# Kernel optimization log

Measured on AMD Instinct MI355X. Metric: run time of the kernel, lower is better.

Reference implementation:

```python
import jax, jax.numpy as jnp
import numpy as np

N = 100000   # nodes
E = 1600000  # edges
F = 128      # input node features
H = 128      # hidden channels
G = 512      # graphs in batch
EPS = 1e-5   # BatchNorm eps


def setup_inputs() -> dict:
    key = jax.random.key(0)
    ks = jax.random.split(key, 24)
    x = jax.random.normal(ks[0], (N, F), jnp.float32)
    edge_index = jax.random.randint(ks[1], (2, E), 0, N)
    batch = jnp.sort(jax.random.randint(ks[2], (N,), 0, G))

    def lin_w(k, i, o):
        return jax.random.normal(k, (i, o), jnp.float32) / np.sqrt(i)

    inp = {
        "x": x, "edge_index": edge_index, "batch": batch,
        "W1": lin_w(ks[3], F, H), "b1": jnp.zeros((H,), jnp.float32),
        "g1": jnp.ones((H,), jnp.float32), "be1": jnp.zeros((H,), jnp.float32),
        "m1": 0.1 * jax.random.normal(ks[4], (H,), jnp.float32),
        "v1": jax.random.uniform(ks[5], (H,), jnp.float32) + 0.5,
        "W2": lin_w(ks[6], H, H), "b2": jnp.zeros((H,), jnp.float32),
        "g2": jnp.ones((H,), jnp.float32), "be2": jnp.zeros((H,), jnp.float32),
        "m2": 0.1 * jax.random.normal(ks[7], (H,), jnp.float32),
        "v2": jax.random.uniform(ks[8], (H,), jnp.float32) + 0.5,
        "W3": lin_w(ks[9], H, H), "b3": jnp.zeros((H,), jnp.float32),
        "g3": jnp.ones((H,), jnp.float32), "be3": jnp.zeros((H,), jnp.float32),
        "m3": 0.1 * jax.random.normal(ks[10], (H,), jnp.float32),
        "v3": jax.random.uniform(ks[11], (H,), jnp.float32) + 0.5,
        "Wl": lin_w(ks[12], H, 1), "bl": jnp.zeros((1,), jnp.float32),
    }
    return inp


def _gcn_norm(edge_index):
    # add self-loops, then symmetric normalization deg^-1/2 A_hat deg^-1/2
    loops = jnp.arange(N)
    src = jnp.concatenate([edge_index[0], loops])
    dst = jnp.concatenate([edge_index[1], loops])
    deg = jax.ops.segment_sum(jnp.ones_like(src, jnp.float32), dst, num_segments=N)
    dinv = jax.lax.rsqrt(jnp.maximum(deg, 1.0))
    norm = dinv[src] * dinv[dst]  # [E+N]
    return src, dst, norm


def _gcn_conv(x, W, b, src, dst, norm):
    h = x @ W                                    # [N,H] dense GEMM first (PyG order)
    msg = h[src] * norm[:, None]                 # gather + scale, [E+N,H]
    agg = jax.ops.segment_sum(msg, dst, num_segments=N)  # scatter-add
    return agg + b


def _bn_relu(x, g, be, m, v):
    # inference BatchNorm1d (running stats) + ReLU
    return jax.nn.relu((x - m) * jax.lax.rsqrt(v + EPS) * g + be)


def reference(x, edge_index, batch,
              W1, b1, g1, be1, m1, v1,
              W2, b2, g2, be2, m2, v2,
              W3, b3, g3, be3, m3, v3,
              Wl, bl):
    src, dst, norm = _gcn_norm(edge_index)
    h = _bn_relu(_gcn_conv(x, W1, b1, src, dst, norm), g1, be1, m1, v1)
    h = _bn_relu(_gcn_conv(h, W2, b2, src, dst, norm), g2, be2, m2, v2)
    h = _bn_relu(_gcn_conv(h, W3, b3, src, dst, norm), g3, be3, m3, v3)
    # global mean pool over graphs
    sums = jax.ops.segment_sum(h, batch, num_segments=G)           # [G,H]
    cnt = jax.ops.segment_sum(jnp.ones((N,), jnp.float32), batch, num_segments=G)
    pooled = sums / jnp.maximum(cnt, 1.0)[:, None]
    # dropout is identity at inference; final linear
    return pooled @ Wl + bl  # [G,1]
```

## Files before the change

kernel.cpp:

```cpp
#include <hip/hip_runtime.h>
#include <hip/hip_bf16.h>

#define NN 100000
#define NE 1600000
#define HD 128
#define NG 512
#define BN_EPS 1e-5f

#define GEMM_BLOCKS 1563
#define HIST_BLOCKS 6250

typedef __attribute__((ext_vector_type(8))) short short8;
typedef __attribute__((ext_vector_type(4))) float floatx4;

__device__ __forceinline__ ushort f2bf(float f) {
    union { float f; uint u; } v; v.f = f;
    uint r = (v.u + 0x7FFF + ((v.u >> 16) & 1)) >> 16;
    return (ushort)r;
}
__device__ __forceinline__ float bflo(uint u) { union { uint u; float f; } v; v.u = u << 16; return v.f; }
__device__ __forceinline__ float bfhi(uint u) { union { uint u; float f; } v; v.u = u & 0xFFFF0000u; return v.f; }

__global__ void k_zero_i(int* p, int n) {
    int i = blockIdx.x * 256 + threadIdx.x;
    if (i < n) p[i] = 0;
}

__global__ void k_prep_w3(const float* __restrict__ W1, const float* __restrict__ W2,
                          const float* __restrict__ W3,
                          ushort* __restrict__ Wt1, ushort* __restrict__ Wt2,
                          ushort* __restrict__ Wt3) {
    int w = blockIdx.x >> 6;
    int i = (blockIdx.x & 63) * 256 + threadIdx.x;
    const float* W = (w == 0) ? W1 : (w == 1) ? W2 : W3;
    ushort* Wt = (w == 0) ? Wt1 : (w == 1) ? Wt2 : Wt3;
    int k = i >> 7, n = i & 127;
    Wt[n * 128 + k] = f2bf(W[i]);
}

__launch_bounds__(256)
__global__ void k_fused1(const float* __restrict__ x, const ushort* __restrict__ Wt,
                         ushort* __restrict__ hs,
                         const int* __restrict__ dst, int* __restrict__ indeg,
                         int* __restrict__ rank) {
    const int tid = threadIdx.x;
    if (blockIdx.x >= GEMM_BLOCKS) {
        int e = (blockIdx.x - GEMM_BLOCKS) * 256 + tid;
        if (e < NE) rank[e] = atomicAdd(&indeg[dst[e]], 1);
        return;
    }
    const int wave = tid >> 6, lane = tid & 63;
    const int m = lane & 15, kg = lane >> 4;
    const long row0 = (long)blockIdx.x * 64 + wave * 16;

    long arow = row0 + m;
    long arc = arow < NN ? arow : (NN - 1);
    const float* xf = x + arc * 128;
    short8 a[4];
#pragma unroll
    for (int s = 0; s < 4; ++s) {
        float4 f0 = *(const float4*)(xf + s * 32 + kg * 8);
        float4 f1 = *(const float4*)(xf + s * 32 + kg * 8 + 4);
        short8 t;
        t[0] = (short)f2bf(f0.x); t[1] = (short)f2bf(f0.y);
        t[2] = (short)f2bf(f0.z); t[3] = (short)f2bf(f0.w);
        t[4] = (short)f2bf(f1.x); t[5] = (short)f2bf(f1.y);
        t[6] = (short)f2bf(f1.z); t[7] = (short)f2bf(f1.w);
        a[s] = t;
    }

    floatx4 acc[8];
#pragma unroll
    for (int ct = 0; ct < 8; ++ct) acc[ct] = (floatx4){0.f, 0.f, 0.f, 0.f};

#pragma unroll
    for (int s = 0; s < 4; ++s) {
#pragma unroll
        for (int ct = 0; ct < 8; ++ct) {
            short8 b = *(const short8*)(Wt + (ct * 16 + m) * 128 + s * 32 + kg * 8);
            acc[ct] = __builtin_amdgcn_mfma_f32_16x16x32_bf16(a[s], b, acc[ct], 0, 0, 0);
        }
    }

#pragma unroll
    for (int r = 0; r < 4; ++r) {
        long orow = row0 + kg * 4 + r;
        if (orow < NN) {
#pragma unroll
            for (int ct = 0; ct < 8; ++ct)
                hs[orow * 128 + ct * 16 + m] = f2bf(acc[ct][r]);
        }
    }
}

__global__ void k_scan1d(const int* __restrict__ indeg, int* __restrict__ rs,
                         int* __restrict__ aux, float* __restrict__ dinv) {
    __shared__ int s[256];
    int t = threadIdx.x;
    int base = blockIdx.x * 1024 + t * 4;
    int v0 = 0, v1 = 0, v2 = 0, v3 = 0;
    if (base + 0 < NN) v0 = indeg[base + 0];
    if (base + 1 < NN) v1 = indeg[base + 1];
    if (base + 2 < NN) v2 = indeg[base + 2];
    if (base + 3 < NN) v3 = indeg[base + 3];
    if (base + 0 < NN) dinv[base + 0] = rsqrtf((float)(v0 + 1));
    if (base + 1 < NN) dinv[base + 1] = rsqrtf((float)(v1 + 1));
    if (base + 2 < NN) dinv[base + 2] = rsqrtf((float)(v2 + 1));
    if (base + 3 < NN) dinv[base + 3] = rsqrtf((float)(v3 + 1));
    int tsum = v0 + v1 + v2 + v3;
    s[t] = tsum;
    __syncthreads();
    for (int o = 1; o < 256; o <<= 1) {
        int x = 0;
        if (t >= o) x = s[t - o];
        __syncthreads();
        s[t] += x;
        __syncthreads();
    }
    int excl = s[t] - tsum;
    if (base + 0 < NN) rs[base + 0] = excl;
    if (base + 1 < NN) rs[base + 1] = excl + v0;
    if (base + 2 < NN) rs[base + 2] = excl + v0 + v1;
    if (base + 3 < NN) rs[base + 3] = excl + v0 + v1 + v2;
    if (t == 255) aux[blockIdx.x] = s[255];
}

__global__ void k_scan2(int* __restrict__ aux, int nblk) {
    __shared__ int s[128];
    int t = threadIdx.x;
    int v = (t < nblk) ? aux[t] : 0;
    s[t] = v;
    __syncthreads();
    for (int o = 1; o < 128; o <<= 1) {
        int x = 0;
        if (t >= o) x = s[t - o];
        __syncthreads();
        s[t] += x;
        __syncthreads();
    }
    if (t < nblk) aux[t] = s[t] - v;
}

__global__ void k_scan3(int* __restrict__ rs, const int* __restrict__ aux) {
    int i = blockIdx.x * 256 + threadIdx.x;
    if (i < NN) rs[i] += aux[i >> 10];
    if (i == 0) rs[NN] = NE;
}

__global__ void k_fill(const int* __restrict__ src, const int* __restrict__ dst,
                       const int* __restrict__ rank, const int* __restrict__ rs,
                       int* __restrict__ csr) {
    int e = blockIdx.x * 256 + threadIdx.x;
    if (e >= NE) return;
    csr[rs[dst[e]] + rank[e]] = src[e];
}

__global__ void k_bn_prep3(const float* __restrict__ b1, const float* __restrict__ g1,
                           const float* __restrict__ be1, const float* __restrict__ m1,
                           const float* __restrict__ v1,
                           const float* __restrict__ b2, const float* __restrict__ g2,
                           const float* __restrict__ be2, const float* __restrict__ m2,
                           const float* __restrict__ v2,
                           const float* __restrict__ b3, const float* __restrict__ g3,
                           const float* __restrict__ be3, const float* __restrict__ m3,
                           const float* __restrict__ v3,
                           float* scale1, float* shift1, float* scale2, float* shift2,
                           float* scale3, float* shift3) {
    int l = blockIdx.x, f = threadIdx.x;
    const float *b, *g, *be, *m, *v;
    float *sc, *sh;
    if (l == 0)      { b = b1; g = g1; be = be1; m = m1; v = v1; sc = scale1; sh = shift1; }
    else if (l == 1) { b = b2; g = g2; be = be2; m = m2; v = v2; sc = scale2; sh = shift2; }
    else             { b = b3; g = g3; be = be3; m = m3; v = v3; sc = scale3; sh = shift3; }
    float s = g[f] * rsqrtf(v[f] + BN_EPS);
    sc[f] = s;
    sh[f] = (b[f] - m[f]) * s + be[f];
}

__global__ void k_gstart(const int* __restrict__ batch, int* __restrict__ gstart) {
    int g = blockIdx.x * 256 + threadIdx.x;
    if (g > NG) return;
    if (g == NG) { gstart[NG] = NN; return; }
    int lo = 0, hi = NN;
    while (lo < hi) {
        int mid = (lo + hi) >> 1;
        if (batch[mid] < g) lo = mid + 1; else hi = mid;
    }
    gstart[g] = lo;
}

#define WT_STRIDE 136
__launch_bounds__(256)
__global__ void k_gemm_l23(const ushort* __restrict__ xb, const ushort* __restrict__ Wt,
                           const float* __restrict__ dinv, ushort* __restrict__ hs) {
    __shared__ ushort sWt[128 * WT_STRIDE];
    const int tid = threadIdx.x;
    for (int i = tid; i < 2048; i += 256) {
        int row = i >> 4, seg = i & 15;
        *(uint4*)&sWt[row * WT_STRIDE + seg * 8] = *(const uint4*)(Wt + row * 128 + seg * 8);
    }
    __syncthreads();

    const int wave = tid >> 6, lane = tid & 63;
    const int m = lane & 15, kg = lane >> 4;
    const long row0 = (long)blockIdx.x * 64 + wave * 16;

    long arow = row0 + m;
    long arc = arow < NN ? arow : (NN - 1);
    short8 a[4];
#pragma unroll
    for (int s = 0; s < 4; ++s)
        a[s] = *(const short8*)(xb + arc * 128 + s * 32 + kg * 8);

    floatx4 acc[8];
#pragma unroll
    for (int ct = 0; ct < 8; ++ct) acc[ct] = (floatx4){0.f, 0.f, 0.f, 0.f};

#pragma unroll
    for (int s = 0; s < 4; ++s) {
#pragma unroll
        for (int ct = 0; ct < 8; ++ct) {
            short8 b = *(const short8*)&sWt[(ct * 16 + m) * WT_STRIDE + s * 32 + kg * 8];
            acc[ct] = __builtin_amdgcn_mfma_f32_16x16x32_bf16(a[s], b, acc[ct], 0, 0, 0);
        }
    }

#pragma unroll
    for (int r = 0; r < 4; ++r) {
        long orow = row0 + kg * 4 + r;
        if (orow < NN) {
            float dd = dinv[orow];
#pragma unroll
            for (int ct = 0; ct < 8; ++ct)
                hs[orow * 128 + ct * 16 + m] = f2bf(acc[ct][r] * dd);
        }
    }
}

template <bool SCALE_SRC>
__global__ void k_gather_bf(const ushort* __restrict__ hs, const int* __restrict__ rs,
                            const int* __restrict__ csr, const float* __restrict__ dinv,
                            const float* __restrict__ scale, const float* __restrict__ shift,
                            ushort* __restrict__ xout) {
    int t = blockIdx.x * 256 + threadIdx.x;
    int d = t >> 4;
    if (d >= NN) return;
    int lane = t & 15;
    int c0 = lane * 8;
    int e0 = rs[d], e1 = rs[d + 1];
    float dd = dinv[d];

    uint4 sv = *(const uint4*)(hs + (long)d * 128 + c0);
    float w = SCALE_SRC ? dd : 1.0f;
    float a0 = w * bflo(sv.x), a1 = w * bfhi(sv.x), a2 = w * bflo(sv.y), a3 = w * bfhi(sv.y);
    float a4 = w * bflo(sv.z), a5 = w * bfhi(sv.z), a6 = w * bflo(sv.w), a7 = w * bfhi(sv.w);

    int j = e0;
    for (; j + 1 < e1; j += 2) {
        int s0 = csr[j], s1 = csr[j + 1];
        uint4 v0 = *(const uint4*)(hs + (long)s0 * 128 + c0);
        uint4 v1 = *(const uint4*)(hs + (long)s1 * 128 + c0);
        if (SCALE_SRC) {
            float w0 = dinv[s0], w1 = dinv[s1];
            a0 += w0 * bflo(v0.x) + w1 * bflo(v1.x);
            a1 += w0 * bfhi(v0.x) + w1 * bfhi(v1.x);
            a2 += w0 * bflo(v0.y) + w1 * bflo(v1.y);
            a3 += w0 * bfhi(v0.y) + w1 * bfhi(v1.y);
            a4 += w0 * bflo(v0.z) + w1 * bflo(v1.z);
            a5 += w0 * bfhi(v0.z) + w1 * bfhi(v1.z);
            a6 += w0 * bflo(v0.w) + w1 * bflo(v1.w);
            a7 += w0 * bfhi(v0.w) + w1 * bfhi(v1.w);
        } else {
            a0 += bflo(v0.x) + bflo(v1.x); a1 += bfhi(v0.x) + bfhi(v1.x);
            a2 += bflo(v0.y) + bflo(v1.y); a3 += bfhi(v0.y) + bfhi(v1.y);
            a4 += bflo(v0.z) + bflo(v1.z); a5 += bfhi(v0.z) + bfhi(v1.z);
            a6 += bflo(v0.w) + bflo(v1.w); a7 += bfhi(v0.w) + bfhi(v1.w);
        }
    }
    if (j < e1) {
        int s0 = csr[j];
        uint4 v0 = *(const uint4*)(hs + (long)s0 * 128 + c0);
        float w0 = SCALE_SRC ? dinv[s0] : 1.0f;
        a0 += w0 * bflo(v0.x); a1 += w0 * bfhi(v0.x);
        a2 += w0 * bflo(v0.y); a3 += w0 * bfhi(v0.y);
        a4 += w0 * bflo(v0.z); a5 += w0 * bfhi(v0.z);
        a6 += w0 * bflo(v0.w); a7 += w0 * bfhi(v0.w);
    }

    float4 sca = *(const float4*)(scale + c0);
    float4 scb = *(const float4*)(scale + c0 + 4);
    float4 sha = *(const float4*)(shift + c0);
    float4 shb = *(const float4*)(shift + c0 + 4);
    float r0 = fmaxf(dd * a0 * sca.x + sha.x, 0.f);
    float r1 = fmaxf(dd * a1 * sca.y + sha.y, 0.f);
    float r2 = fmaxf(dd * a2 * sca.z + sha.z, 0.f);
    float r3 = fmaxf(dd * a3 * sca.w + sha.w, 0.f);
    float r4 = fmaxf(dd * a4 * scb.x + shb.x, 0.f);
    float r5 = fmaxf(dd * a5 * scb.y + shb.y, 0.f);
    float r6 = fmaxf(dd * a6 * scb.z + shb.z, 0.f);
    float r7 = fmaxf(dd * a7 * scb.w + shb.w, 0.f);
    uint4 o;
    o.x = (uint)f2bf(r0) | ((uint)f2bf(r1) << 16);
    o.y = (uint)f2bf(r2) | ((uint)f2bf(r3) << 16);
    o.z = (uint)f2bf(r4) | ((uint)f2bf(r5) << 16);
    o.w = (uint)f2bf(r6) | ((uint)f2bf(r7) << 16);
    *(uint4*)(xout + (long)d * 128 + c0) = o;
}

__global__ void k_pool_final2(const ushort* __restrict__ x, const int* __restrict__ gstart,
                              const float* __restrict__ Wl, const float* __restrict__ bl,
                              float* __restrict__ out) {
    __shared__ float red[256];
    int g = blockIdx.x;
    int tid = threadIdx.x;
    int f = tid & 127;
    int half = tid >> 7;
    int i0 = gstart[g], i1 = gstart[g + 1];

    float acc = 0.f;
    for (int i = i0 + half; i < i1; i += 2) {
        union { uint u; float f; } v; v.u = (uint)x[(long)i * 128 + f] << 16;
        acc += v.f;
    }
    red[tid] = acc;
    __syncthreads();
    if (tid < 128) red[tid] = (red[tid] + red[tid + 128]) * Wl[tid];
    __syncthreads();
    for (int o = 64; o > 0; o >>= 1) {
        if (tid < o) red[tid] += red[tid + o];
        __syncthreads();
    }
    if (tid == 0) out[g] = red[0] / fmaxf((float)(i1 - i0), 1.f) + bl[0];
}

extern "C" void kernel_launch(void* const* d_in, const int* in_sizes, int n_in,
                              void* d_out, int out_size, void* d_ws, size_t ws_size,
                              hipStream_t stream) {
    const float* x   = (const float*)d_in[0];
    const int*   ei  = (const int*)d_in[1];
    const int*   bat = (const int*)d_in[2];
    const float* W1  = (const float*)d_in[3];
    const float* b1  = (const float*)d_in[4];
    const float* g1  = (const float*)d_in[5];
    const float* be1 = (const float*)d_in[6];
    const float* m1  = (const float*)d_in[7];
    const float* v1  = (const float*)d_in[8];
    const float* W2  = (const float*)d_in[9];
    const float* b2  = (const float*)d_in[10];
    const float* g2  = (const float*)d_in[11];
    const float* be2 = (const float*)d_in[12];
    const float* m2  = (const float*)d_in[13];
    const float* v2  = (const float*)d_in[14];
    const float* W3  = (const float*)d_in[15];
    const float* b3  = (const float*)d_in[16];
    const float* g3  = (const float*)d_in[17];
    const float* be3 = (const float*)d_in[18];
    const float* m3  = (const float*)d_in[19];
    const float* v3  = (const float*)d_in[20];
    const float* Wl  = (const float*)d_in[21];
    const float* bl  = (const float*)d_in[22];
    float* out = (float*)d_out;

    const int* srcp = ei;
    const int* dstp = ei + NE;

    char* ws = (char*)d_ws;
    size_t off = 0;
    auto alloc = [&](size_t bytes) { char* p = ws + off; off += (bytes + 255) & ~255ULL; return p; };
    float*  dinv   = (float*) alloc(NN * 4);
    int*    indeg  = (int*)   alloc(NN * 4);
    int*    rs     = (int*)   alloc((NN + 1) * 4);
    int*    aux    = (int*)   alloc(128 * 4);
    int*    csr    = (int*)   alloc(NE * 4);
    int*    rank   = (int*)   alloc(NE * 4);
    float*  scale1 = (float*) alloc(HD * 4);
    float*  shift1 = (float*) alloc(HD * 4);
    float*  scale2 = (float*) alloc(HD * 4);
    float*  shift2 = (float*) alloc(HD * 4);
    float*  scale3 = (float*) alloc(HD * 4);
    float*  shift3 = (float*) alloc(HD * 4);
    int*    gstart = (int*)   alloc((NG + 1) * 4);
    ushort* Wt1    = (ushort*)alloc(128 * 128 * 2);
    ushort* Wt2    = (ushort*)alloc(128 * 128 * 2);
    ushort* Wt3    = (ushort*)alloc(128 * 128 * 2);
    ushort* hs     = (ushort*)alloc((size_t)NN * HD * 2);
    ushort* xbuf   = (ushort*)alloc((size_t)NN * HD * 2);

    const int nblk_scan = (NN + 1023) / 1024;
    const int grid_n    = (NN + 255) / 256;
    const int grid_e    = (NE + 255) / 256;
    const int gath_grid = (NN * 16 + 255) / 256;

    k_zero_i<<<grid_n, 256, 0, stream>>>(indeg, NN);
    k_prep_w3<<<192, 256, 0, stream>>>(W1, W2, W3, Wt1, Wt2, Wt3);

    k_fused1<<<GEMM_BLOCKS + HIST_BLOCKS, 256, 0, stream>>>(x, Wt1, hs, dstp, indeg, rank);

    k_scan1d<<<nblk_scan, 256, 0, stream>>>(indeg, rs, aux, dinv);
    k_scan2<<<1, 128, 0, stream>>>(aux, nblk_scan);
    k_scan3<<<grid_n, 256, 0, stream>>>(rs, aux);
    k_fill<<<grid_e, 256, 0, stream>>>(srcp, dstp, rank, rs, csr);

    k_bn_prep3<<<3, 128, 0, stream>>>(b1, g1, be1, m1, v1, b2, g2, be2, m2, v2,
                                      b3, g3, be3, m3, v3,
                                      scale1, shift1, scale2, shift2, scale3, shift3);
    k_gstart<<<3, 256, 0, stream>>>(bat, gstart);

    k_gather_bf<true><<<gath_grid, 256, 0, stream>>>(hs, rs, csr, dinv, scale1, shift1, xbuf);
    k_gemm_l23<<<GEMM_BLOCKS, 256, 0, stream>>>(xbuf, Wt2, dinv, hs);
    k_gather_bf<false><<<gath_grid, 256, 0, stream>>>(hs, rs, csr, dinv, scale2, shift2, xbuf);
    k_gemm_l23<<<GEMM_BLOCKS, 256, 0, stream>>>(xbuf, Wt3, dinv, hs);
    k_gather_bf<false><<<gath_grid, 256, 0, stream>>>(hs, rs, csr, dinv, scale3, shift3, xbuf);

    k_pool_final2<<<NG, 256, 0, stream>>>(xbuf, gstart, Wl, bl, out);
}
```

Measured before the change: 530.0 us.

## Split degree histogram per XCD and gather each node with a full wave

The in-degree histogram now keeps one copy per XCD, selected through the hardware XCC id, and uses workgroup-scope relaxed atomics to reduce cross-die atomic contention. Each edge's rank carries its XCD id in the top byte, and the scan pass turns the per-XCD counts into per-XCD offsets for the CSR fill. The aggregation kernel now assigns one 64-lane wave per destination node: four 16-lane sub-groups walk interleaved edges with index prefetching, then combine partial sums with cross-lane shuffles. This adds more atomic memory and scan work, and relies on workgroup-scope atomics staying correct across CUs that share an XCD's L2.

```diff
diff --git a/kernel.cpp b/kernel.cpp
--- a/kernel.cpp
+++ b/kernel.cpp
@@ -6,6 +6,7 @@
 #define HD 128
 #define NG 512
 #define BN_EPS 1e-5f
+#define NXCD 8
 
 #define GEMM_BLOCKS 1563
 #define HIST_BLOCKS 6250
@@ -20,6 +21,10 @@
 }
 __device__ __forceinline__ float bflo(uint u) { union { uint u; float f; } v; v.u = u << 16; return v.f; }
 __device__ __forceinline__ float bfhi(uint u) { union { uint u; float f; } v; v.u = u & 0xFFFF0000u; return v.f; }
+
+__device__ __forceinline__ uint xcc_id() {
+    return (uint)__builtin_amdgcn_s_getreg(20 | (31 << 11)) & (NXCD - 1);
+}
 
 __global__ void k_zero_i(int* p, int n) {
     int i = blockIdx.x * 256 + threadIdx.x;
@@ -46,7 +51,13 @@
     const int tid = threadIdx.x;
     if (blockIdx.x >= GEMM_BLOCKS) {
         int e = (blockIdx.x - GEMM_BLOCKS) * 256 + tid;
-        if (e < NE) rank[e] = atomicAdd(&indeg[dst[e]], 1);
+        if (e < NE) {
+            uint xc = xcc_id();
+            int d = dst[e];
+            int lr = __hip_atomic_fetch_add(&indeg[xc * NN + d], 1,
+                                            __ATOMIC_RELAXED, __HIP_MEMORY_SCOPE_WORKGROUP);
+            rank[e] = (int)((xc << 24) | (uint)lr);
+        }
         return;
     }
     const int wave = tid >> 6, lane = tid & 63;
@@ -99,10 +110,14 @@
     int t = threadIdx.x;
     int base = blockIdx.x * 1024 + t * 4;
     int v0 = 0, v1 = 0, v2 = 0, v3 = 0;
-    if (base + 0 < NN) v0 = indeg[base + 0];
-    if (base + 1 < NN) v1 = indeg[base + 1];
-    if (base + 2 < NN) v2 = indeg[base + 2];
-    if (base + 3 < NN) v3 = indeg[base + 3];
+#pragma unroll
+    for (int xc = 0; xc < NXCD; ++xc) {
+        const int* p = indeg + xc * NN;
+        if (base + 0 < NN) v0 += p[base + 0];
+        if (base + 1 < NN) v1 += p[base + 1];
+        if (base + 2 < NN) v2 += p[base + 2];
+        if (base + 3 < NN) v3 += p[base + 3];
+    }
     if (base + 0 < NN) dinv[base + 0] = rsqrtf((float)(v0 + 1));
     if (base + 1 < NN) dinv[base + 1] = rsqrtf((float)(v1 + 1));
     if (base + 2 < NN) dinv[base + 2] = rsqrtf((float)(v2 + 1));
@@ -141,18 +156,32 @@
     if (t < nblk) aux[t] = s[t] - v;
 }
 
-__global__ void k_scan3(int* __restrict__ rs, const int* __restrict__ aux) {
+__global__ void k_scan3(int* __restrict__ rs, const int* __restrict__ aux,
+                        int* __restrict__ indeg) {
     int i = blockIdx.x * 256 + threadIdx.x;
-    if (i < NN) rs[i] += aux[i >> 10];
+    if (i < NN) {
+        int b = rs[i] + aux[i >> 10];
+        rs[i] = b;
+        int run = b;
+#pragma unroll
+        for (int xc = 0; xc < NXCD; ++xc) {
+            int c = indeg[xc * NN + i];
+            indeg[xc * NN + i] = run;
+            run += c;
+        }
+    }
     if (i == 0) rs[NN] = NE;
 }
 
 __global__ void k_fill(const int* __restrict__ src, const int* __restrict__ dst,
-                       const int* __restrict__ rank, const int* __restrict__ rs,
+                       const int* __restrict__ rank, const int* __restrict__ indeg,
                        int* __restrict__ csr) {
     int e = blockIdx.x * 256 + threadIdx.x;
     if (e >= NE) return;
-    csr[rs[dst[e]] + rank[e]] = src[e];
+    uint r = (uint)rank[e];
+    int xc = (int)(r >> 24);
+    int lr = (int)(r & 0xFFFFFFu);
+    csr[indeg[xc * NN + dst[e]] + lr] = src[e];
 }
 
 __global__ void k_bn_prep3(const float* __restrict__ b1, const float* __restrict__ g1,
@@ -238,73 +267,94 @@
 }
 
 template <bool SCALE_SRC>
-__global__ void k_gather_bf(const ushort* __restrict__ hs, const int* __restrict__ rs,
-                            const int* __restrict__ csr, const float* __restrict__ dinv,
-                            const float* __restrict__ scale, const float* __restrict__ shift,
-                            ushort* __restrict__ xout) {
-    int t = blockIdx.x * 256 + threadIdx.x;
-    int d = t >> 4;
-    if (d >= NN) return;
-    int lane = t & 15;
-    int c0 = lane * 8;
-    int e0 = rs[d], e1 = rs[d + 1];
-    float dd = dinv[d];
-
-    uint4 sv = *(const uint4*)(hs + (long)d * 128 + c0);
-    float w = SCALE_SRC ? dd : 1.0f;
-    float a0 = w * bflo(sv.x), a1 = w * bfhi(sv.x), a2 = w * bflo(sv.y), a3 = w * bfhi(sv.y);
-    float a4 = w * bflo(sv.z), a5 = w * bfhi(sv.z), a6 = w * bflo(sv.w), a7 = w * bfhi(sv.w);
-
-    int j = e0;
-    for (; j + 1 < e1; j += 2) {
-        int s0 = csr[j], s1 = csr[j + 1];
+__launch_bounds__(256)
+__global__ void k_gather_w(const ushort* __restrict__ hs, const int* __restrict__ rs,
+                           const int* __restrict__ csr, const float* __restrict__ dinv,
+                           const float* __restrict__ scale, const float* __restrict__ shift,
+                           ushort* __restrict__ xout) {
+    const int tid = threadIdx.x;
+    const int d = blockIdx.x * 4 + (tid >> 6);
+    const int lane = tid & 63;
+    const int sub = lane >> 4;
+    const int c0 = (lane & 15) * 8;
+
+    const int e0 = rs[d], e1 = rs[d + 1];
+    const float dd = dinv[d];
+
+    float a0 = 0.f, a1 = 0.f, a2 = 0.f, a3 = 0.f,
+          a4 = 0.f, a5 = 0.f, a6 = 0.f, a7 = 0.f;
+
+    if (sub == 0) {
+        uint4 sv = *(const uint4*)(hs + (long)d * 128 + c0);
+        float w = SCALE_SRC ? dd : 1.0f;
+        a0 = w * bflo(sv.x); a1 = w * bfhi(sv.x);
+        a2 = w * bflo(sv.y); a3 = w * bfhi(sv.y);
+        a4 = w * bflo(sv.z); a5 = w * bfhi(sv.z);
+        a6 = w * bflo(sv.w); a7 = w * bfhi(sv.w);
+    }
+
+    int j = e0 + sub;
+    int s0 = 0, s1 = 0;
+    bool have = (j < e1 - 4);
+    if (have) { s0 = csr[j]; s1 = csr[j + 4]; }
+    while (have) {
+        int jn = j + 8;
+        bool nxt = (jn < e1 - 4);
+        int n0 = 0, n1 = 0;
+        if (nxt) { n0 = csr[jn]; n1 = csr[jn + 4]; }
+        float w0 = SCALE_SRC ? dinv[s0] : 1.0f;
+        float w1 = SCALE_SRC ? dinv[s1] : 1.0f;
         uint4 v0 = *(const uint4*)(hs + (long)s0 * 128 + c0);
         uint4 v1 = *(const uint4*)(hs + (long)s1 * 128 + c0);
-        if (SCALE_SRC) {
-            float w0 = dinv[s0], w1 = dinv[s1];
-            a0 += w0 * bflo(v0.x) + w1 * bflo(v1.x);
-            a1 += w0 * bfhi(v0.x) + w1 * bfhi(v1.x);
-            a2 += w0 * bflo(v0.y) + w1 * bflo(v1.y);
-            a3 += w0 * bfhi(v0.y) + w1 * bfhi(v1.y);
-            a4 += w0 * bflo(v0.z) + w1 * bflo(v1.z);
-            a5 += w0 * bfhi(v0.z) + w1 * bfhi(v1.z);
-            a6 += w0 * bflo(v0.w) + w1 * bflo(v1.w);
-            a7 += w0 * bfhi(v0.w) + w1 * bfhi(v1.w);
-        } else {
-            a0 += bflo(v0.x) + bflo(v1.x); a1 += bfhi(v0.x) + bfhi(v1.x);
-            a2 += bflo(v0.y) + bflo(v1.y); a3 += bfhi(v0.y) + bfhi(v1.y);
-            a4 += bflo(v0.z) + bflo(v1.z); a5 += bfhi(v0.z) + bfhi(v1.z);
-            a6 += bflo(v0.w) + bflo(v1.w); a7 += bfhi(v0.w) + bfhi(v1.w);
-        }
+        a0 += w0 * bflo(v0.x) + w1 * bflo(v1.x);
+        a1 += w0 * bfhi(v0.x) + w1 * bfhi(v1.x);
+        a2 += w0 * bflo(v0.y) + w1 * bflo(v1.y);
+        a3 += w0 * bfhi(v0.y) + w1 * bfhi(v1.y);
+        a4 += w0 * bflo(v0.z) + w1 * bflo(v1.z);
+        a5 += w0 * bfhi(v0.z) + w1 * bfhi(v1.z);
+        a6 += w0 * bflo(v0.w) + w1 * bflo(v1.w);
+        a7 += w0 * bfhi(v0.w) + w1 * bfhi(v1.w);
+        j = jn; s0 = n0; s1 = n1; have = nxt;
     }
     if (j < e1) {
-        int s0 = csr[j];
-        uint4 v0 = *(const uint4*)(hs + (long)s0 * 128 + c0);
-        float w0 = SCALE_SRC ? dinv[s0] : 1.0f;
-        a0 += w0 * bflo(v0.x); a1 += w0 * bfhi(v0.x);
-        a2 += w0 * bflo(v0.y); a3 += w0 * bfhi(v0.y);
-        a4 += w0 * bflo(v0.z); a5 += w0 * bfhi(v0.z);
-        a6 += w0 * bflo(v0.w); a7 += w0 * bfhi(v0.w);
-    }
-
-    float4 sca = *(const float4*)(scale + c0);
-    float4 scb = *(const float4*)(scale + c0 + 4);
-    float4 sha = *(const float4*)(shift + c0);
-    float4 shb = *(const float4*)(shift + c0 + 4);
-    float r0 = fmaxf(dd * a0 * sca.x + sha.x, 0.f);
-    float r1 = fmaxf(dd * a1 * sca.y + sha.y, 0.f);
-    float r2 = fmaxf(dd * a2 * sca.z + sha.z, 0.f);
-    float r3 = fmaxf(dd * a3 * sca.w + sha.w, 0.f);
-    float r4 = fmaxf(dd * a4 * scb.x + shb.x, 0.f);
-    float r5 = fmaxf(dd * a5 * scb.y + shb.y, 0.f);
-    float r6 = fmaxf(dd * a6 * scb.z + shb.z, 0.f);
-    float r7 = fmaxf(dd * a7 * scb.w + shb.w, 0.f);
-    uint4 o;
-    o.x = (uint)f2bf(r0) | ((uint)f2bf(r1) << 16);
-    o.y = (uint)f2bf(r2) | ((uint)f2bf(r3) << 16);
-    o.z = (uint)f2bf(r4) | ((uint)f2bf(r5) << 16);
-    o.w = (uint)f2bf(r6) | ((uint)f2bf(r7) << 16);
-    *(uint4*)(xout + (long)d * 128 + c0) = o;
+        int sx = csr[j];
+        float wx = SCALE_SRC ? dinv[sx] : 1.0f;
+        uint4 v0 = *(const uint4*)(hs + (long)sx * 128 + c0);
+        a0 += wx * bflo(v0.x); a1 += wx * bfhi(v0.x);
+        a2 += wx * bflo(v0.y); a3 += wx * bfhi(v0.y);
+        a4 += wx * bflo(v0.z); a5 += wx * bfhi(v0.z);
+        a6 += wx * bflo(v0.w); a7 += wx * bfhi(v0.w);
+    }
+
+    a0 += __shfl_xor(a0, 16); a1 += __shfl_xor(a1, 16);
+    a2 += __shfl_xor(a2, 16); a3 += __shfl_xor(a3, 16);
+    a4 += __shfl_xor(a4, 16); a5 += __shfl_xor(a5, 16);
+    a6 += __shfl_xor(a6, 16); a7 += __shfl_xor(a7, 16);
+    a0 += __shfl_xor(a0, 32); a1 += __shfl_xor(a1, 32);
+    a2 += __shfl_xor(a2, 32); a3 += __shfl_xor(a3, 32);
+    a4 += __shfl_xor(a4, 32); a5 += __shfl_xor(a5, 32);
+    a6 += __shfl_xor(a6, 32); a7 += __shfl_xor(a7, 32);
+
+    if (sub == 0) {
+        float4 sca = *(const float4*)(scale + c0);
+        float4 scb = *(const float4*)(scale + c0 + 4);
+        float4 sha = *(const float4*)(shift + c0);
+        float4 shb = *(const float4*)(shift + c0 + 4);
+        float r0 = fmaxf(dd * a0 * sca.x + sha.x, 0.f);
+        float r1 = fmaxf(dd * a1 * sca.y + sha.y, 0.f);
+        float r2 = fmaxf(dd * a2 * sca.z + sha.z, 0.f);
+        float r3 = fmaxf(dd * a3 * sca.w + sha.w, 0.f);
+        float r4 = fmaxf(dd * a4 * scb.x + shb.x, 0.f);
+        float r5 = fmaxf(dd * a5 * scb.y + shb.y, 0.f);
+        float r6 = fmaxf(dd * a6 * scb.z + shb.z, 0.f);
+        float r7 = fmaxf(dd * a7 * scb.w + shb.w, 0.f);
+        uint4 o;
+        o.x = (uint)f2bf(r0) | ((uint)f2bf(r1) << 16);
+        o.y = (uint)f2bf(r2) | ((uint)f2bf(r3) << 16);
+        o.z = (uint)f2bf(r4) | ((uint)f2bf(r5) << 16);
+        o.w = (uint)f2bf(r6) | ((uint)f2bf(r7) << 16);
+        *(uint4*)(xout + (long)d * 128 + c0) = o;
+    }
 }
 
 __global__ void k_pool_final2(const ushort* __restrict__ x, const int* __restrict__ gstart,
@@ -368,7 +418,7 @@
     size_t off = 0;
     auto alloc = [&](size_t bytes) { char* p = ws + off; off += (bytes + 255) & ~255ULL; return p; };
     float*  dinv   = (float*) alloc(NN * 4);
-    int*    indeg  = (int*)   alloc(NN * 4);
+    int*    indeg  = (int*)   alloc((size_t)NXCD * NN * 4);
     int*    rs     = (int*)   alloc((NN + 1) * 4);
     int*    aux    = (int*)   alloc(128 * 4);
     int*    csr    = (int*)   alloc(NE * 4);
@@ -389,28 +439,28 @@
     const int nblk_scan = (NN + 1023) / 1024;
     const int grid_n    = (NN + 255) / 256;
     const int grid_e    = (NE + 255) / 256;
-    const int gath_grid = (NN * 16 + 255) / 256;
-
-    k_zero_i<<<grid_n, 256, 0, stream>>>(indeg, NN);
+    const int gath_grid = NN / 4;
+
+    k_zero_i<<<(NXCD * NN + 255) / 256, 256, 0, stream>>>(indeg, NXCD * NN);
     k_prep_w3<<<192, 256, 0, stream>>>(W1, W2, W3, Wt1, Wt2, Wt3);
 
     k_fused1<<<GEMM_BLOCKS + HIST_BLOCKS, 256, 0, stream>>>(x, Wt1, hs, dstp, indeg, rank);
 
     k_scan1d<<<nblk_scan, 256, 0, stream>>>(indeg, rs, aux, dinv);
     k_scan2<<<1, 128, 0, stream>>>(aux, nblk_scan);
-    k_scan3<<<grid_n, 256, 0, stream>>>(rs, aux);
-    k_fill<<<grid_e, 256, 0, stream>>>(srcp, dstp, rank, rs, csr);
+    k_scan3<<<grid_n, 256, 0, stream>>>(rs, aux, indeg);
+    k_fill<<<grid_e, 256, 0, stream>>>(srcp, dstp, rank, indeg, csr);
 
     k_bn_prep3<<<3, 128, 0, stream>>>(b1, g1, be1, m1, v1, b2, g2, be2, m2, v2,
                                       b3, g3, be3, m3, v3,
                                       scale1, shift1, scale2, shift2, scale3, shift3);
     k_gstart<<<3, 256, 0, stream>>>(bat, gstart);
 
-    k_gather_bf<true><<<gath_grid, 256, 0, stream>>>(hs, rs, csr, dinv, scale1, shift1, xbuf);
+    k_gather_w<true><<<gath_grid, 256, 0, stream>>>(hs, rs, csr, dinv, scale1, shift1, xbuf);
     k_gemm_l23<<<GEMM_BLOCKS, 256, 0, stream>>>(xbuf, Wt2, dinv, hs);
-    k_gather_bf<false><<<gath_grid, 256, 0, stream>>>(hs, rs, csr, dinv, scale2, shift2, xbuf);
+    k_gather_w<false><<<gath_grid, 256, 0, stream>>>(hs, rs, csr, dinv, scale2, shift2, xbuf);
     k_gemm_l23<<<GEMM_BLOCKS, 256, 0, stream>>>(xbuf, Wt3, dinv, hs);
-    k_gather_bf<false><<<gath_grid, 256, 0, stream>>>(hs, rs, csr, dinv, scale3, shift3, xbuf);
+    k_gather_w<false><<<gath_grid, 256, 0, stream>>>(hs, rs, csr, dinv, scale3, shift3, xbuf);
 
     k_pool_final2<<<NG, 256, 0, stream>>>(xbuf, gstart, Wl, bl, out);
 }
```

Result: no change. 524.8 us (-1.0%).
